# Performance work log

Hardware: AMD Instinct MI355X
Metric: run time of the kernel (lower is better)

## Reference

```python
import jax, jax.numpy as jnp
import numpy as np

B, L, H, NH = 4, 1024, 768, 12
NE, M, P = 30, 6, 600
EMB, BS, NC = 768, 16, 97
NEG = -1e30


def setup_inputs() -> dict:
    key = jax.random.key(0)
    ks = jax.random.split(key, 9)
    sequence_output = jax.random.normal(ks[0], (B, L, H), jnp.float32)
    attention = jax.random.uniform(ks[1], (B, NH, L, L), jnp.float32)
    mention_idx = jax.random.randint(ks[2], (B, NE, M), 0, L)
    mention_mask = jnp.ones((B, NE, M), jnp.float32)
    hts = jax.random.randint(ks[3], (B, P, 2), 0, NE)
    s = 0.02
    head_W = jax.random.normal(ks[4], (EMB, 2 * H), jnp.float32) * s
    head_b = jnp.zeros((EMB,), jnp.float32)
    tail_W = jax.random.normal(ks[5], (EMB, 2 * H), jnp.float32) * s
    tail_b = jnp.zeros((EMB,), jnp.float32)
    proj_W = jax.random.normal(ks[6], (H, EMB * BS), jnp.float32) * s
    cls_W = jax.random.normal(ks[7], (NC, H), jnp.float32) * s
    cls_b = jnp.zeros((NC,), jnp.float32)
    return {
        'sequence_output': sequence_output, 'attention': attention,
        'head_W': head_W, 'head_b': head_b, 'tail_W': tail_W, 'tail_b': tail_b,
        'proj_W': proj_W, 'cls_W': cls_W, 'cls_b': cls_b,
        'mention_mask': mention_mask, 'mention_idx': mention_idx, 'hts': hts,
    }


def reference(sequence_output, attention, head_W, head_b, tail_W, tail_b,
              proj_W, cls_W, cls_b, mention_mask, mention_idx, hts):
    b_, l_, h_ = sequence_output.shape
    bidx = jnp.arange(b_)[:, None, None]                     # [B,1,1]
    # ---- per-entity pooling (segment reduce over ragged mentions) ----
    m_emb = sequence_output[bidx, mention_idx]               # [B,NE,M,H]
    att_t = attention.transpose(0, 2, 1, 3)                  # [B,L,NH,L]
    m_att = att_t[bidx, mention_idx]                         # [B,NE,M,NH,L]
    masked = jnp.where(mention_mask[..., None] > 0, m_emb, NEG)
    e_emb = jax.nn.logsumexp(masked, axis=2)                 # [B,NE,H]
    cnt = jnp.maximum(mention_mask.sum(2), 1.0)              # [B,NE]
    e_att = (m_att * mention_mask[..., None, None]).sum(2) / cnt[..., None, None]  # [B,NE,NH,L]
    # ---- head/tail gathers over pairs ----
    b2 = jnp.arange(b_)[:, None]                             # [B,1]
    h_emb = e_emb[b2, hts[..., 0]]                           # [B,P,H]
    t_emb = e_emb[b2, hts[..., 1]]
    h_att = e_att[b2, hts[..., 0]]                           # [B,P,NH,L]
    t_att = e_att[b2, hts[..., 1]]
    ht_att = (h_att * t_att).mean(2)                         # [B,P,L]
    ht_att = ht_att / (ht_att.sum(-1, keepdims=True) + 1e-30)
    rs = jnp.einsum('bpl,blh->bph', ht_att, sequence_output) # [B,P,H]
    # ---- extractors + block-bilinear classifier ----
    hs = jnp.tanh(jnp.concatenate([h_emb, rs], -1) @ head_W.T + head_b)  # [B,P,EMB]
    ts = jnp.tanh(jnp.concatenate([t_emb, rs], -1) @ tail_W.T + tail_b)
    emb = hs.shape[-1]
    bs = proj_W.shape[1] // emb
    p_ = hs.shape[1]
    b1 = hs.reshape(b_, p_, emb // bs, bs)
    b2t = ts.reshape(b_, p_, emb // bs, bs)
    bl = (b1[..., :, None] * b2t[..., None, :]).reshape(b_, p_, emb * bs)
    logits = (bl @ proj_W.T) @ cls_W.T + cls_b               # [B,P,NC]
    return logits
```

## Files before the change

kernel.cpp:

```cpp
#include <hip/hip_runtime.h>
#include <cmath>

#define B_   4
#define L_   1024
#define H_   768
#define NH_  12
#define NE_  30
#define M_   6
#define P_   600
#define EMB_ 768
#define BS_  16
#define NC_  97

typedef __bf16 bf16x8 __attribute__((ext_vector_type(8)));
typedef float floatx4 __attribute__((ext_vector_type(4)));

union V16 { uint4 q; __bf16 b[8]; bf16x8 v; };
union V8  { unsigned long long u; __bf16 b[4]; };

__device__ __forceinline__ void gload16(const __bf16* g, __bf16* l) {
  __builtin_amdgcn_global_load_lds(
      (const __attribute__((address_space(1))) void*)g,
      (__attribute__((address_space(3))) void*)l, 16, 0, 0);
}

__device__ __forceinline__ void gemm_core(
    const __bf16* __restrict__ A, int lda, long aRow0,
    const __bf16* __restrict__ Bt, int ldb, long bRow0,
    int K, __bf16* sm, floatx4 acc[2][2])
{
  const int tid = threadIdx.x;
  const int lid = tid & 63, w = tid >> 6;
  const int ar = (w & 1) * 32, bc = (w >> 1) * 32;
  const int frow = lid & 15, kg = lid >> 4;
  const int grow = tid >> 2, gq = (tid & 3) * 8;
  const __bf16* ag = A + (aRow0 + grow) * (long)lda + gq;
  const __bf16* bg = Bt + (bRow0 + grow) * (long)ldb + gq;
  {
    __bf16* wbase = sm + w * 512;
    gload16(ag, wbase);
    gload16(bg, wbase + 2048);
  }
  __syncthreads();
  int cur = 0;
  for (int k0 = 0; k0 < K; k0 += 32) {
    __bf16* As = sm + cur * 4096;
    __bf16* Bs = As + 2048;
    if (k0 + 32 < K) {
      __bf16* An = sm + (cur ^ 1) * 4096 + w * 512;
      gload16(ag + k0 + 32, An);
      gload16(bg + k0 + 32, An + 2048);
    }
    V16 a0, a1, b0, b1;
    a0.q = *reinterpret_cast<const uint4*>(As + (ar + frow) * 32 + kg * 8);
    a1.q = *reinterpret_cast<const uint4*>(As + (ar + 16 + frow) * 32 + kg * 8);
    b0.q = *reinterpret_cast<const uint4*>(Bs + (bc + frow) * 32 + kg * 8);
    b1.q = *reinterpret_cast<const uint4*>(Bs + (bc + 16 + frow) * 32 + kg * 8);
    acc[0][0] = __builtin_amdgcn_mfma_f32_16x16x32_bf16(a0.v, b0.v, acc[0][0], 0, 0, 0);
    acc[0][1] = __builtin_amdgcn_mfma_f32_16x16x32_bf16(a0.v, b1.v, acc[0][1], 0, 0, 0);
    acc[1][0] = __builtin_amdgcn_mfma_f32_16x16x32_bf16(a1.v, b0.v, acc[1][0], 0, 0, 0);
    acc[1][1] = __builtin_amdgcn_mfma_f32_16x16x32_bf16(a1.v, b1.v, acc[1][1], 0, 0, 0);
    __syncthreads();
    cur ^= 1;
  }
}

#define S1_CVT  2400
#define S1_TPW  9216
#define S1_TPS  3072
#define S1_POOL 120
#define S1_ATT  1440

__device__ __forceinline__ void transpose_body(
    const float* __restrict__ in, __bf16* __restrict__ out,
    int R, int C, int bx, int by, float (*t)[33])
{
  int c0 = bx*32, r0 = by*32;
  int tx = threadIdx.x & 31, ty = threadIdx.x >> 5;
#pragma unroll
  for (int p = 0; p < 4; ++p)
    t[ty + p*8][tx] = in[(long)(r0 + ty + p*8)*C + c0 + tx];
  __syncthreads();
#pragma unroll
  for (int p = 0; p < 4; ++p)
    out[(long)(c0 + ty + p*8)*R + r0 + tx] = (__bf16)t[tx][ty + p*8];
}

__global__ __launch_bounds__(256) void k_prep(
    const float* __restrict__ seq, const float* __restrict__ att,
    const float* __restrict__ headW, const float* __restrict__ tailW,
    const float* __restrict__ projW, const float* __restrict__ clsW,
    const float* __restrict__ mmask, const int* __restrict__ midx,
    __bf16* __restrict__ Wt, __bf16* __restrict__ clsA,
    __bf16* __restrict__ projWT, __bf16* __restrict__ seqT,
    __bf16* __restrict__ e_embB, __bf16* __restrict__ e_att)
{
  __shared__ float t[32][33];
  int blk = blockIdx.x;
  int tid = threadIdx.x;
  if (blk < S1_CVT) {
    int gid = blk*256 + tid;
    if (gid < 2*H_*384) {
      int sel = gid / (H_*384);
      int rem = gid % (H_*384);
      int o = rem / 384;
      int k4 = (rem % 384) * 4;
      const float* W = sel ? tailW : headW;
      float4 v = *reinterpret_cast<const float4*>(W + (long)o*(2*H_) + k4);
      V8 d; d.b[0]=(__bf16)v.x; d.b[1]=(__bf16)v.y; d.b[2]=(__bf16)v.z; d.b[3]=(__bf16)v.w;
      *reinterpret_cast<unsigned long long*>(Wt + ((long)sel*H_ + o)*(2*H_) + k4) = d.u;
    } else {
      int rem = gid - 2*H_*384;
      int row = rem / 192;
      int k4 = (rem % 192) * 4;
      V8 d;
      if (row < NC_) {
        float4 v = *reinterpret_cast<const float4*>(clsW + (long)row*H_ + k4);
        d.b[0]=(__bf16)v.x; d.b[1]=(__bf16)v.y; d.b[2]=(__bf16)v.z; d.b[3]=(__bf16)v.w;
      } else {
        d.b[0]=d.b[1]=d.b[2]=d.b[3]=(__bf16)0.f;
      }
      *reinterpret_cast<unsigned long long*>(clsA + (long)row*H_ + k4) = d.u;
    }
  } else if (blk < S1_CVT + S1_TPW) {
    int b = blk - S1_CVT;
    transpose_body(projW, projWT, H_, EMB_*BS_, b % 384, b / 384, t);
  } else if (blk < S1_CVT + S1_TPW + S1_TPS) {
    int b = blk - (S1_CVT + S1_TPW);
    int bx = b % 24, by = (b / 24) % 32, bz = b / (24*32);
    transpose_body(seq + (long)bz*L_*H_, seqT + (long)bz*H_*L_, L_, H_, bx, by, t);
  } else if (blk < S1_CVT + S1_TPW + S1_TPS + S1_POOL) {
    int be = blk - (S1_CVT + S1_TPW + S1_TPS);
    int idx[M_]; float msk[M_];
#pragma unroll
    for (int m = 0; m < M_; ++m) {
      idx[m] = midx[be * M_ + m];
      msk[m] = mmask[be * M_ + m];
    }
    int b = be / NE_;
    const float* sb = seq + (size_t)b * L_ * H_;
    for (int h = tid; h < H_; h += 256) {
      float v[M_]; float mx = -3.0e38f;
#pragma unroll
      for (int m = 0; m < M_; ++m) {
        float x = (msk[m] > 0.f) ? sb[(size_t)idx[m] * H_ + h] : -1e30f;
        v[m] = x; mx = fmaxf(mx, x);
      }
      float s = 0.f;
#pragma unroll
      for (int m = 0; m < M_; ++m) s += expf(v[m] - mx);
      e_embB[(size_t)be * H_ + h] = (__bf16)(mx + logf(s));
    }
  } else {
    int i = (blk - (S1_CVT + S1_TPW + S1_TPS + S1_POOL))*256 + tid;
    int l4 = (i & 255) * 4;
    int nh = (i >> 8) % NH_;
    int be = i / (256 * NH_);
    int b  = be / NE_;
    float s0=0.f, s1=0.f, s2=0.f, s3=0.f, cnt=0.f;
#pragma unroll
    for (int m = 0; m < M_; ++m) {
      float mk = mmask[be*M_ + m];
      cnt += mk;
      int id = midx[be*M_ + m];
      float4 a = *reinterpret_cast<const float4*>(
          att + (((size_t)b*NH_ + nh)*L_ + id)*L_ + l4);
      s0 += mk*a.x; s1 += mk*a.y; s2 += mk*a.z; s3 += mk*a.w;
    }
    float inv = 1.f / fmaxf(cnt, 1.f);
    V8 o;
    o.b[0]=(__bf16)(s0*inv); o.b[1]=(__bf16)(s1*inv);
    o.b[2]=(__bf16)(s2*inv); o.b[3]=(__bf16)(s3*inv);
    *reinterpret_cast<unsigned long long*>(e_att + ((size_t)be*NH_ + nh)*L_ + l4) = o.u;
  }
}

#define S2_WC  384
#define S2_PRE 48
#define S2_HT  2400

__global__ __launch_bounds__(256) void k_mid(
    const __bf16* __restrict__ clsA, const __bf16* __restrict__ projWT,
    const __bf16* __restrict__ e_att, const int* __restrict__ hts,
    const __bf16* __restrict__ e_embB, const __bf16* __restrict__ Wt,
    __bf16* __restrict__ WcT, __bf16* __restrict__ htatt,
    float* __restrict__ hpre, float* __restrict__ tpre)
{
  __shared__ __bf16 sm[2*4096];
  int blk = blockIdx.x;
  int tid = threadIdx.x;
  if (blk < S2_WC) {
    int n0 = (blk % 192)*64, r0 = (blk / 192)*64;
    floatx4 acc[2][2] = {};
    gemm_core(clsA, H_, r0, projWT, H_, n0, H_, sm, acc);
    int lid = tid & 63, w = tid >> 6;
    int ar = (w&1)*32, bc = (w>>1)*32, frow = lid&15, kg = lid>>4;
#pragma unroll
    for (int i = 0; i < 2; ++i)
#pragma unroll
      for (int r = 0; r < 4; ++r) {
        int c = r0 + ar + i*16 + kg*4 + r;
#pragma unroll
        for (int j = 0; j < 2; ++j)
          WcT[(long)c*(EMB_*BS_) + n0 + bc + j*16 + frow] = (__bf16)acc[i][j][r];
      }
  } else if (blk < S2_WC + S2_PRE) {
    int tb = blk - S2_WC;
    int o0 = (tb % 12)*64;
    int r0 = ((tb / 12) & 1)*64;
    int sel = tb / 24;
    floatx4 acc[2][2] = {};
    gemm_core(e_embB, H_, r0, Wt + (long)sel*H_*(2*H_), 2*H_, o0, H_, sm, acc);
    float* out = sel ? tpre : hpre;
    int lid = tid & 63, w = tid >> 6;
    int ar = (w&1)*32, bc = (w>>1)*32, frow = lid&15, kg = lid>>4;
#pragma unroll
    for (int i = 0; i < 2; ++i)
#pragma unroll
      for (int r = 0; r < 4; ++r) {
        int be = r0 + ar + i*16 + kg*4 + r;
        if (be < B_*NE_) {
#pragma unroll
          for (int j = 0; j < 2; ++j)
            out[(long)be*EMB_ + o0 + bc + j*16 + frow] = acc[i][j][r];
        }
      }
  } else {
    int bp = blk - (S2_WC + S2_PRE);
    int b = bp / P_;
    int hi = hts[bp*2 + 0], ti = hts[bp*2 + 1];
    const __bf16* ha = e_att + (size_t)(b*NE_ + hi) * NH_ * L_;
    const __bf16* ta = e_att + (size_t)(b*NE_ + ti) * NH_ * L_;
    int l4 = tid * 4;
    float v[4] = {0.f,0.f,0.f,0.f};
#pragma unroll
    for (int nh = 0; nh < NH_; ++nh) {
      V8 x, y;
      x.u = *reinterpret_cast<const unsigned long long*>(ha + nh*L_ + l4);
      y.u = *reinterpret_cast<const unsigned long long*>(ta + nh*L_ + l4);
#pragma unroll
      for (int q = 0; q < 4; ++q) v[q] += (float)x.b[q] * (float)y.b[q];
    }
    float loc = 0.f;
#pragma unroll
    for (int q = 0; q < 4; ++q) { v[q] *= (1.f/NH_); loc += v[q]; }
    float* red = reinterpret_cast<float*>(sm);
    for (int off = 32; off > 0; off >>= 1) loc += __shfl_down(loc, off, 64);
    if ((tid & 63) == 0) red[tid >> 6] = loc;
    __syncthreads();
    float inv = 1.f / (red[0] + red[1] + red[2] + red[3] + 1e-30f);
    V8 o;
#pragma unroll
    for (int q = 0; q < 4; ++q) o.b[q] = (__bf16)(v[q] * inv);
    *reinterpret_cast<unsigned long long*>(htatt + (size_t)bp*L_ + l4) = o.u;
  }
}

__global__ __launch_bounds__(256) void k_rs_mfma(
    const __bf16* __restrict__ htatt, const __bf16* __restrict__ seqT,
    __bf16* __restrict__ rs)
{
  __shared__ __bf16 sm[2*4096];
  int b = blockIdx.z, p0 = blockIdx.y*64, h0 = blockIdx.x*64;
  floatx4 acc[2][2] = {};
  gemm_core(htatt, L_, (long)b*P_ + p0, seqT + (long)b*H_*L_, L_, h0, L_, sm, acc);
  int lid = threadIdx.x & 63, w = threadIdx.x >> 6;
  int ar = (w&1)*32, bc = (w>>1)*32, frow = lid&15, kg = lid>>4;
#pragma unroll
  for (int i = 0; i < 2; ++i)
#pragma unroll
    for (int r = 0; r < 4; ++r) {
      int p = p0 + ar + i*16 + kg*4 + r;
      if (p < P_) {
#pragma unroll
        for (int j = 0; j < 2; ++j)
          rs[((long)b*P_ + p)*H_ + h0 + bc + j*16 + frow] = (__bf16)acc[i][j][r];
      }
    }
}

__global__ __launch_bounds__(256) void k_extract_mfma(
    const __bf16* __restrict__ rs, const __bf16* __restrict__ Wt,
    const float* __restrict__ headb, const float* __restrict__ tailb,
    const float* __restrict__ hpre, const float* __restrict__ tpre,
    const int* __restrict__ hts, __bf16* __restrict__ hs, __bf16* __restrict__ ts)
{
  __shared__ __bf16 sm[2*4096];
  int sel = blockIdx.z, r0 = blockIdx.y*64, o0 = blockIdx.x*64;
  const float* bias = sel ? tailb : headb;
  const float* pre = sel ? tpre : hpre;
  __bf16* out = sel ? ts : hs;
  floatx4 acc[2][2] = {};
  gemm_core(rs, H_, r0, Wt + (long)sel*H_*(2*H_) + H_, 2*H_, o0, H_, sm, acc);
  int lid = threadIdx.x & 63, w = threadIdx.x >> 6;
  int ar = (w&1)*32, bc = (w>>1)*32, frow = lid&15, kg = lid>>4;
#pragma unroll
  for (int i = 0; i < 2; ++i)
#pragma unroll
    for (int r = 0; r < 4; ++r) {
      int row = r0 + ar + i*16 + kg*4 + r;
      if (row < B_*P_) {
        int b = row / P_;
        int e = hts[row*2 + sel];
        const float* prow = pre + (long)(b*NE_ + e) * EMB_;
#pragma unroll
        for (int j = 0; j < 2; ++j) {
          int o = o0 + bc + j*16 + frow;
          out[(long)row*EMB_ + o] = (__bf16)tanhf(acc[i][j][r] + prow[o] + bias[o]);
        }
      }
    }
}

__global__ __launch_bounds__(512) void k_logits_mfma(
    const __bf16* __restrict__ hs, const __bf16* __restrict__ ts,
    const __bf16* __restrict__ WcT, const float* __restrict__ clsb,
    float* __restrict__ out)
{
  int r0 = (blockIdx.x >> 2) * 16;
  int ks = blockIdx.x & 3;
  int tid = threadIdx.x;
  int w = tid >> 6, lid = tid & 63;
  int frow = lid & 15, kg = lid >> 4;
  int row = r0 + frow;
  long hsrow = (long)row * EMB_;
  floatx4 acc[7] = {};
  int kbase0 = ks*3072 + w*384;
  for (int s = 0; s < 12; ++s) {
    int kb = kbase0 + s*32 + kg*8;
    int q16 = (kb >> 8) << 4;
    int ii = (kb >> 4) & 15;
    int jj0 = kb & 15;
    float hv = (float)hs[hsrow + q16 + ii];
    V16 tsv; tsv.q = *reinterpret_cast<const uint4*>(ts + hsrow + q16 + jj0);
    bf16x8 af;
#pragma unroll
    for (int j = 0; j < 8; ++j) af[j] = (__bf16)(hv * (float)tsv.b[j]);
#pragma unroll
    for (int f = 0; f < 7; ++f) {
      V16 bv; bv.q = *reinterpret_cast<const uint4*>(WcT + (long)(f*16 + frow)*(EMB_*BS_) + kb);
      acc[f] = __builtin_amdgcn_mfma_f32_16x16x32_bf16(af, bv.v, acc[f], 0, 0, 0);
    }
  }
  __shared__ float red[8][16][112];
#pragma unroll
  for (int f = 0; f < 7; ++f)
#pragma unroll
    for (int r = 0; r < 4; ++r)
      red[w][kg*4 + r][f*16 + frow] = acc[f][r];
  __syncthreads();
  for (int e = tid; e < 16*112; e += 512) {
    int rr = e / 112, cc = e % 112;
    if (cc < NC_) {
      float s = (ks == 0) ? clsb[cc] : 0.f;
#pragma unroll
      for (int ww = 0; ww < 8; ++ww) s += red[ww][rr][cc];
      atomicAdd(out + (long)(r0 + rr)*NC_ + cc, s);
    }
  }
}

extern "C" void kernel_launch(void* const* d_in, const int* in_sizes, int n_in,
                              void* d_out, int out_size, void* d_ws, size_t ws_size,
                              hipStream_t stream) {
  const float* seq   = (const float*)d_in[0];
  const float* att   = (const float*)d_in[1];
  const float* headW = (const float*)d_in[2];
  const float* headb = (const float*)d_in[3];
  const float* tailW = (const float*)d_in[4];
  const float* tailb = (const float*)d_in[5];
  const float* projW = (const float*)d_in[6];
  const float* clsW  = (const float*)d_in[7];
  const float* clsb  = (const float*)d_in[8];
  const float* mmask = (const float*)d_in[9];
  const int* midx = (const int*)d_in[10];
  const int* hts  = (const int*)d_in[11];

  char* p = (char*)d_ws;
  auto alloc_f = [&](size_t n){ float* r = (float*)p; p += n*sizeof(float); return r; };
  auto alloc_b = [&](size_t n){ __bf16* r = (__bf16*)p; p += n*2; return r; };
  float* hpre    = alloc_f((size_t)B_*NE_*EMB_);
  float* tpre    = alloc_f((size_t)B_*NE_*EMB_);
  __bf16* e_embB = alloc_b((size_t)128*H_);
  __bf16* e_att  = alloc_b((size_t)B_*NE_*NH_*L_);
  __bf16* htattb = alloc_b((size_t)2464*L_);
  __bf16* seqT   = alloc_b((size_t)B_*H_*L_);
  __bf16* rsb    = alloc_b((size_t)2432*H_);
  __bf16* Wt     = alloc_b((size_t)2*H_*2*H_);
  __bf16* clsA   = alloc_b((size_t)128*H_);
  __bf16* WcT    = alloc_b((size_t)128*EMB_*BS_);
  __bf16* projWT = alloc_b((size_t)EMB_*BS_*H_);
  __bf16* hsb = projWT;
  __bf16* tsb = projWT + (size_t)B_*P_*EMB_;

  hipMemsetAsync(d_out, 0, (size_t)B_*P_*NC_*sizeof(float), stream);

  k_prep<<<S1_CVT + S1_TPW + S1_TPS + S1_POOL + S1_ATT, 256, 0, stream>>>(
      seq, att, headW, tailW, projW, clsW, mmask, midx,
      Wt, clsA, projWT, seqT, e_embB, e_att);
  k_mid<<<S2_WC + S2_PRE + S2_HT, 256, 0, stream>>>(
      clsA, projWT, e_att, hts, e_embB, Wt, WcT, htattb, hpre, tpre);
  k_rs_mfma<<<dim3(H_/64, 10, B_), 256, 0, stream>>>(htattb, seqT, rsb);
  k_extract_mfma<<<dim3(EMB_/64, 38, 2), 256, 0, stream>>>(
      rsb, Wt, headb, tailb, hpre, tpre, hts, hsb, tsb);
  k_logits_mfma<<<600, 512, 0, stream>>>(hsb, tsb, WcT, clsb, (float*)d_out);
}
```

Measured before the change: 423.8 us.

## Triple-buffer GEMM core with vmcnt waits and halve classifier reduction LDS

The shared MFMA GEMM core moves from a double-buffered loop with two __syncthreads per step to a three-stage LDS ring. It prefetches two K tiles ahead and uses s_waitcnt vmcnt(2) plus a single barrier per iteration, so global-to-LDS loads overlap more with MFMA work. GEMM kernels grow their LDS from 16KB to 24KB, which may reduce occupancy. Separately, the classifier reduction buffer is halved: the upper four waves accumulate into the lower four slots after an extra barrier, cutting LDS use at the cost of one more sync.

```diff
diff --git a/kernel.cpp b/kernel.cpp
--- a/kernel.cpp
+++ b/kernel.cpp
@@ -24,6 +24,21 @@
       (__attribute__((address_space(3))) void*)l, 16, 0, 0);
 }
 
+__device__ __forceinline__ void mfma_step(
+    const __bf16* As, const __bf16* Bs,
+    int ar, int bc, int frow, int kg, floatx4 acc[2][2])
+{
+  V16 a0, a1, b0, b1;
+  a0.q = *reinterpret_cast<const uint4*>(As + (ar + frow) * 32 + kg * 8);
+  a1.q = *reinterpret_cast<const uint4*>(As + (ar + 16 + frow) * 32 + kg * 8);
+  b0.q = *reinterpret_cast<const uint4*>(Bs + (bc + frow) * 32 + kg * 8);
+  b1.q = *reinterpret_cast<const uint4*>(Bs + (bc + 16 + frow) * 32 + kg * 8);
+  acc[0][0] = __builtin_amdgcn_mfma_f32_16x16x32_bf16(a0.v, b0.v, acc[0][0], 0, 0, 0);
+  acc[0][1] = __builtin_amdgcn_mfma_f32_16x16x32_bf16(a0.v, b1.v, acc[0][1], 0, 0, 0);
+  acc[1][0] = __builtin_amdgcn_mfma_f32_16x16x32_bf16(a1.v, b0.v, acc[1][0], 0, 0, 0);
+  acc[1][1] = __builtin_amdgcn_mfma_f32_16x16x32_bf16(a1.v, b1.v, acc[1][1], 0, 0, 0);
+}
+
 __device__ __forceinline__ void gemm_core(
     const __bf16* __restrict__ A, int lda, long aRow0,
     const __bf16* __restrict__ Bt, int ldb, long bRow0,
@@ -36,33 +51,32 @@
   const int grow = tid >> 2, gq = (tid & 3) * 8;
   const __bf16* ag = A + (aRow0 + grow) * (long)lda + gq;
   const __bf16* bg = Bt + (bRow0 + grow) * (long)ldb + gq;
-  {
-    __bf16* wbase = sm + w * 512;
-    gload16(ag, wbase);
-    gload16(bg, wbase + 2048);
+  __bf16* wA = sm + w * 512;
+  const int nt = K >> 5;
+  gload16(ag, wA);
+  gload16(bg, wA + 2048);
+  gload16(ag + 32, wA + 4096);
+  gload16(bg + 32, wA + 4096 + 2048);
+  int cur = 0;
+  for (int i = 0; i < nt - 1; ++i) {
+    asm volatile("s_waitcnt vmcnt(2)" ::: "memory");
+    __builtin_amdgcn_s_barrier();
+    __builtin_amdgcn_sched_barrier(0);
+    if (i + 2 < nt) {
+      int nb = cur + 2; if (nb >= 3) nb -= 3;
+      __bf16* d = sm + nb * 4096 + w * 512;
+      gload16(ag + (i + 2) * 32, d);
+      gload16(bg + (i + 2) * 32, d + 2048);
+    }
+    const __bf16* As = sm + cur * 4096;
+    mfma_step(As, As + 2048, ar, bc, frow, kg, acc);
+    cur += 1; if (cur == 3) cur = 0;
   }
-  __syncthreads();
-  int cur = 0;
-  for (int k0 = 0; k0 < K; k0 += 32) {
-    __bf16* As = sm + cur * 4096;
-    __bf16* Bs = As + 2048;
-    if (k0 + 32 < K) {
-      __bf16* An = sm + (cur ^ 1) * 4096 + w * 512;
-      gload16(ag + k0 + 32, An);
-      gload16(bg + k0 + 32, An + 2048);
-    }
-    V16 a0, a1, b0, b1;
-    a0.q = *reinterpret_cast<const uint4*>(As + (ar + frow) * 32 + kg * 8);
-    a1.q = *reinterpret_cast<const uint4*>(As + (ar + 16 + frow) * 32 + kg * 8);
-    b0.q = *reinterpret_cast<const uint4*>(Bs + (bc + frow) * 32 + kg * 8);
-    b1.q = *reinterpret_cast<const uint4*>(Bs + (bc + 16 + frow) * 32 + kg * 8);
-    acc[0][0] = __builtin_amdgcn_mfma_f32_16x16x32_bf16(a0.v, b0.v, acc[0][0], 0, 0, 0);
-    acc[0][1] = __builtin_amdgcn_mfma_f32_16x16x32_bf16(a0.v, b1.v, acc[0][1], 0, 0, 0);
-    acc[1][0] = __builtin_amdgcn_mfma_f32_16x16x32_bf16(a1.v, b0.v, acc[1][0], 0, 0, 0);
-    acc[1][1] = __builtin_amdgcn_mfma_f32_16x16x32_bf16(a1.v, b1.v, acc[1][1], 0, 0, 0);
-    __syncthreads();
-    cur ^= 1;
-  }
+  asm volatile("s_waitcnt vmcnt(0)" ::: "memory");
+  __builtin_amdgcn_s_barrier();
+  __builtin_amdgcn_sched_barrier(0);
+  const __bf16* As = sm + cur * 4096;
+  mfma_step(As, As + 2048, ar, bc, frow, kg, acc);
 }
 
 #define S1_CVT  2400
@@ -186,7 +200,7 @@
     __bf16* __restrict__ WcT, __bf16* __restrict__ htatt,
     float* __restrict__ hpre, float* __restrict__ tpre)
 {
-  __shared__ __bf16 sm[2*4096];
+  __shared__ __bf16 sm[3*4096];
   int blk = blockIdx.x;
   int tid = threadIdx.x;
   if (blk < S2_WC) {
@@ -260,7 +274,7 @@
     const __bf16* __restrict__ htatt, const __bf16* __restrict__ seqT,
     __bf16* __restrict__ rs)
 {
-  __shared__ __bf16 sm[2*4096];
+  __shared__ __bf16 sm[3*4096];
   int b = blockIdx.z, p0 = blockIdx.y*64, h0 = blockIdx.x*64;
   floatx4 acc[2][2] = {};
   gemm_core(htatt, L_, (long)b*P_ + p0, seqT + (long)b*H_*L_, L_, h0, L_, sm, acc);
@@ -285,7 +299,7 @@
     const float* __restrict__ hpre, const float* __restrict__ tpre,
     const int* __restrict__ hts, __bf16* __restrict__ hs, __bf16* __restrict__ ts)
 {
-  __shared__ __bf16 sm[2*4096];
+  __shared__ __bf16 sm[3*4096];
   int sel = blockIdx.z, r0 = blockIdx.y*64, o0 = blockIdx.x*64;
   const float* bias = sel ? tailb : headb;
   const float* pre = sel ? tpre : hpre;
@@ -342,19 +356,27 @@
       acc[f] = __builtin_amdgcn_mfma_f32_16x16x32_bf16(af, bv.v, acc[f], 0, 0, 0);
     }
   }
-  __shared__ float red[8][16][112];
+  __shared__ float red[4][16][112];
 #pragma unroll
   for (int f = 0; f < 7; ++f)
 #pragma unroll
-    for (int r = 0; r < 4; ++r)
-      red[w][kg*4 + r][f*16 + frow] = acc[f][r];
+    for (int r = 0; r < 4; ++r) {
+      if (w < 4) red[w][kg*4 + r][f*16 + frow] = acc[f][r];
+    }
+  __syncthreads();
+#pragma unroll
+  for (int f = 0; f < 7; ++f)
+#pragma unroll
+    for (int r = 0; r < 4; ++r) {
+      if (w >= 4) red[w-4][kg*4 + r][f*16 + frow] += acc[f][r];
+    }
   __syncthreads();
   for (int e = tid; e < 16*112; e += 512) {
     int rr = e / 112, cc = e % 112;
     if (cc < NC_) {
       float s = (ks == 0) ? clsb[cc] : 0.f;
 #pragma unroll
-      for (int ww = 0; ww < 8; ++ww) s += red[ww][rr][cc];
+      for (int ww = 0; ww < 4; ++ww) s += red[ww][rr][cc];
       atomicAdd(out + (long)(r0 + rr)*NC_ + cc, s);
     }
   }
```

Result: no change. 420.4 us (-0.8%).
